# Optimization experiments

Measured on AMD Instinct MI355X. Metric: run time of the kernel, lower is better.

The kernel has to match this reference:

```python
import jax, jax.numpy as jnp
import numpy as np

B, N, D, H = 2, 2048, 1024, 16
DH = D // H  # 64


def setup_inputs() -> dict:
    key = jax.random.key(0)
    k1, k2, k3, k4, k5 = jax.random.split(key, 5)
    x = jax.random.normal(k1, (B, N, D), dtype=jnp.float32)
    # per-head kqv Linear weights, stacked: [H, D, 3*DH] (acts as x @ W)
    W_kqv = jax.random.normal(k2, (H, D, 3 * DH), dtype=jnp.float32) * 0.02
    b_kqv = jax.random.normal(k3, (H, 3 * DH), dtype=jnp.float32) * 0.02
    W_proj = jax.random.normal(k4, (D, D), dtype=jnp.float32) * 0.02
    b_proj = jax.random.normal(k5, (D,), dtype=jnp.float32) * 0.02
    return {"x": x, "W_kqv": W_kqv, "b_kqv": b_kqv, "W_proj": W_proj, "b_proj": b_proj}


def reference(x, W_kqv, b_kqv, W_proj, b_proj):
    # per-head projections, all heads batched: [B, H, N, 3*DH]
    kqv = jnp.einsum('bnd,hde->bhne', x, W_kqv) + b_kqv[None, :, None, :]
    # original chunk order is k, q, v
    k, q, v = jnp.split(kqv, 3, axis=-1)  # each [B, H, N, DH]
    # scores: A = q @ k^T / sqrt(DH)  -> [B, H, N, N]
    A = jnp.einsum('bhnd,bhmd->bhnm', q, k) / jnp.sqrt(jnp.asarray(DH, x.dtype))
    causal = jnp.tril(jnp.ones((N, N), dtype=bool))
    A = jnp.where(causal[None, None, :, :], A, -jnp.inf)
    attn = jax.nn.softmax(A, axis=-1)
    sa = jnp.einsum('bhnm,bhmd->bhnd', attn, v)          # [B, H, N, DH]
    sa = sa.transpose(0, 2, 1, 3).reshape(B, N, D)        # concat heads
    out = sa @ W_proj.T + b_proj                          # output projection
    return out
```

## Files before the change

kernel.cpp:

```cpp
#include <hip/hip_runtime.h>
#include <hip/hip_bf16.h>
#include <cstdint>
#include <cstddef>

#define B_  2
#define N_  2048
#define D_  1024
#define H_  16
#define DH_ 64
#define E3_ 192

typedef __attribute__((ext_vector_type(8))) short short8;
typedef __attribute__((ext_vector_type(8))) unsigned short ushort8v;
typedef __attribute__((ext_vector_type(4))) float floatx4;

static __device__ __forceinline__ unsigned short f2bf(float f) {
  union { float f; unsigned u; } c; c.f = f;
  unsigned r = c.u + 0x7fffu + ((c.u >> 16) & 1u);
  return (unsigned short)(r >> 16);
}

#define MFMA(a,b,c) __builtin_amdgcn_mfma_f32_16x16x32_bf16((a),(b),(c),0,0,0)

#define GL_LDS16(g, l) __builtin_amdgcn_global_load_lds( \
    (const __attribute__((address_space(1))) void*)(g),  \
    (__attribute__((address_space(3))) void*)(l), 16, 0, 0)

__global__ __launch_bounds__(256) void k_f2bf(const float* __restrict__ in,
                                              unsigned short* __restrict__ out, int n8) {
  int i = blockIdx.x * blockDim.x + threadIdx.x;
  if (i >= n8) return;
  const float4* p = (const float4*)in + (size_t)i * 2;
  float4 a = p[0], b = p[1];
  ushort8v o;
  o[0]=f2bf(a.x); o[1]=f2bf(a.y); o[2]=f2bf(a.z); o[3]=f2bf(a.w);
  o[4]=f2bf(b.x); o[5]=f2bf(b.y); o[6]=f2bf(b.z); o[7]=f2bf(b.w);
  *((ushort8v*)out + i) = o;
}

__global__ __launch_bounds__(256) void k_twkqv(const float* __restrict__ W,
                                               unsigned short* __restrict__ Wt) {
  __shared__ float tile[64][65];
  int h = blockIdx.z, e0 = blockIdx.y * 64, d0 = blockIdx.x * 64;
  int t = threadIdx.x;
  const float* Wp = W + (size_t)h * D_ * E3_;
  int dr = t >> 2, ec = (t & 3) * 16;
#pragma unroll
  for (int j = 0; j < 16; j += 4) {
    float4 wv = *(const float4*)&Wp[(size_t)(d0 + dr) * E3_ + e0 + ec + j];
    tile[dr][ec + j + 0] = wv.x; tile[dr][ec + j + 1] = wv.y;
    tile[dr][ec + j + 2] = wv.z; tile[dr][ec + j + 3] = wv.w;
  }
  __syncthreads();
  int er = t >> 2, dc = (t & 3) * 16;
  ushort8v o0, o1;
#pragma unroll
  for (int j = 0; j < 8; j++) o0[j] = f2bf(tile[dc + j][er]);
#pragma unroll
  for (int j = 0; j < 8; j++) o1[j] = f2bf(tile[dc + 8 + j][er]);
  size_t o = ((size_t)h * E3_ + e0 + er) * D_ + d0 + dc;
  *(ushort8v*)&Wt[o]     = o0;
  *(ushort8v*)&Wt[o + 8] = o1;
}

__global__ __launch_bounds__(256) void k_qkv(const unsigned short* __restrict__ Xb,
                                             const unsigned short* __restrict__ Wt,
                                             const float* __restrict__ bkqv,
                                             unsigned short* __restrict__ Qb,
                                             unsigned short* __restrict__ Kb,
                                             unsigned short* __restrict__ Vt) {
  __shared__ unsigned short Alds[128 * 32];
  __shared__ unsigned short Blds[128 * 32];
  int t = threadIdx.x;
  int m0 = blockIdx.x * 128, c0 = blockIdx.y * 128;
  int wave = t >> 6, lane = t & 63, quad = lane >> 4, l16 = lane & 15;
  int wm = (wave >> 1) * 64, wn = (wave & 1) * 64;
  floatx4 acc[4][4];
#pragma unroll
  for (int i = 0; i < 4; i++)
#pragma unroll
    for (int j = 0; j < 4; j++) acc[i][j] = (floatx4){0.f, 0.f, 0.f, 0.f};

  const unsigned short* gA = Xb + (size_t)(m0 + wave * 32 + (lane >> 2)) * D_ + (lane & 3) * 8;
  const unsigned short* gB = Wt + (size_t)(c0 + wave * 32 + (lane >> 2)) * D_ + (lane & 3) * 8;
  unsigned short* lA = &Alds[(wave * 32) * 32];
  unsigned short* lB = &Blds[(wave * 32) * 32];

  for (int k0 = 0; k0 < D_; k0 += 32) {
    GL_LDS16(gA + k0,            lA);
    GL_LDS16(gA + k0 + 16 * D_,  lA + 16 * 32);
    GL_LDS16(gB + k0,            lB);
    GL_LDS16(gB + k0 + 16 * D_,  lB + 16 * 32);
    __syncthreads();
    short8 a[4], b[4];
#pragma unroll
    for (int mi = 0; mi < 4; mi++) a[mi] = *(const short8*)&Alds[(wm + mi * 16 + l16) * 32 + quad * 8];
#pragma unroll
    for (int ni = 0; ni < 4; ni++) b[ni] = *(const short8*)&Blds[(wn + ni * 16 + l16) * 32 + quad * 8];
#pragma unroll
    for (int mi = 0; mi < 4; mi++)
#pragma unroll
      for (int ni = 0; ni < 4; ni++) acc[mi][ni] = MFMA(a[mi], b[ni], acc[mi][ni]);
    __syncthreads();
  }

#pragma unroll
  for (int mi = 0; mi < 4; mi++)
#pragma unroll
    for (int ni = 0; ni < 4; ni++) {
      int col = c0 + wn + ni * 16 + l16;
      int h = col / 192;
      int e = col - h * 192;
      int grow = m0 + wm + mi * 16 + quad * 4;
      int b = grow >> 11, n0 = grow & (N_ - 1);
      int bh = b * H_ + h;
      float bias = bkqv[col];
      floatx4 v = acc[mi][ni];
      if (e < 64) {
        size_t base = ((size_t)bh * N_ + n0) * DH_ + e;
#pragma unroll
        for (int r = 0; r < 4; r++) Kb[base + (size_t)r * DH_] = f2bf(v[r] + bias);
      } else if (e < 128) {
        size_t base = ((size_t)bh * N_ + n0) * DH_ + (e - 64);
#pragma unroll
        for (int r = 0; r < 4; r++) Qb[base + (size_t)r * DH_] = f2bf((v[r] + bias) * 0.125f);
      } else {
        ushort4 pk;
        pk.x = f2bf(v[0] + bias); pk.y = f2bf(v[1] + bias);
        pk.z = f2bf(v[2] + bias); pk.w = f2bf(v[3] + bias);
        *(ushort4*)&Vt[((size_t)bh * DH_ + (e - 128)) * N_ + n0] = pk;
      }
    }
}

#define PSTR 72
__global__ __launch_bounds__(256) void k_flash(const unsigned short* __restrict__ Qb,
                                               const unsigned short* __restrict__ Kb,
                                               const unsigned short* __restrict__ Vt,
                                               unsigned short* __restrict__ sab) {
  int bh = blockIdx.x;
  int yr = blockIdx.y, g = yr >> 3, o = yr & 7;
  int qb = (g == 0) ? o : (g == 1) ? 31 - o : (g == 2) ? 8 + o : 23 - o;
  int q0b = qb * 64;
  int wave = threadIdx.x >> 6;
  int lane = threadIdx.x & 63, quad = lane >> 4, l16 = lane & 15;
  const unsigned short* Qp = Qb + (size_t)bh * N_ * DH_;
  const unsigned short* Kp = Kb + (size_t)bh * N_ * DH_;
  const unsigned short* Vp = Vt + (size_t)bh * DH_ * N_;
  __shared__ unsigned short Klds[2 * 64 * 32];
  __shared__ unsigned short Vlds[2 * 64 * 32];
  __shared__ unsigned short Plds[4][16 * PSTR];
  unsigned short* P = Plds[wave];

  int q0w = q0b + wave * 16;
  short8 qf0 = *(const short8*)&Qp[(q0w + l16) * DH_ + quad * 8];
  short8 qf1 = *(const short8*)&Qp[(q0w + l16) * DH_ + 32 + quad * 8];

  const unsigned short* gK = Kp + (size_t)(wave * 16 + (lane >> 2)) * DH_ + (lane & 3) * 8;
  const unsigned short* gV = Vp + (size_t)(wave * 16 + (lane >> 2)) * N_ + (lane & 3) * 8;
  unsigned short* lK = &Klds[(wave * 16) * 32];
  unsigned short* lV = &Vlds[(wave * 16) * 32];

  floatx4 O[4];
  float lr[4];
#pragma unroll
  for (int r = 0; r < 4; r++) { O[r] = (floatx4){0.f, 0.f, 0.f, 0.f}; lr[r] = 0.f; }

  for (int kv0 = 0; kv0 <= q0b; kv0 += 64) {
    GL_LDS16(gK + (size_t)kv0 * DH_,      lK);
    GL_LDS16(gK + (size_t)kv0 * DH_ + 32, lK + 64 * 32);
    GL_LDS16(gV + kv0,                    lV);
    GL_LDS16(gV + kv0 + 32,               lV + 64 * 32);
    __syncthreads();

    short8 kf[4][2], vf[4][2];
#pragma unroll
    for (int c = 0; c < 4; c++) {
      kf[c][0] = *(const short8*)&Klds[(c * 16 + l16) * 32 + quad * 8];
      kf[c][1] = *(const short8*)&Klds[(64 + c * 16 + l16) * 32 + quad * 8];
    }
#pragma unroll
    for (int dt = 0; dt < 4; dt++) {
      vf[dt][0] = *(const short8*)&Vlds[(dt * 16 + l16) * 32 + quad * 8];
      vf[dt][1] = *(const short8*)&Vlds[(64 + dt * 16 + l16) * 32 + quad * 8];
    }
    floatx4 s[4];
#pragma unroll
    for (int c = 0; c < 4; c++) {
      s[c] = (floatx4){0.f, 0.f, 0.f, 0.f};
      s[c] = MFMA(qf0, kf[c][0], s[c]);
      s[c] = MFMA(qf1, kf[c][1], s[c]);
    }
    if (kv0 == q0b) {
#pragma unroll
      for (int c = 0; c < 4; c++)
#pragma unroll
        for (int r = 0; r < 4; r++) {
          int row = wave * 16 + quad * 4 + r;
          if (c * 16 + l16 > row) s[c][r] = -1e30f;
        }
    }
#pragma unroll
    for (int c = 0; c < 4; c++)
#pragma unroll
      for (int r = 0; r < 4; r++)
        s[c][r] = __builtin_amdgcn_exp2f(s[c][r] * 1.44269504f);
#pragma unroll
    for (int r = 0; r < 4; r++)
      lr[r] += (s[0][r] + s[1][r]) + (s[2][r] + s[3][r]);
#pragma unroll
    for (int c = 0; c < 4; c++)
#pragma unroll
      for (int r = 0; r < 4; r++)
        P[(quad * 4 + r) * PSTR + c * 16 + l16] = f2bf(s[c][r]);
    __asm__ volatile("s_waitcnt lgkmcnt(0)" ::: "memory");
    short8 pa0 = *(const short8*)&P[l16 * PSTR + quad * 8];
    short8 pa1 = *(const short8*)&P[l16 * PSTR + 32 + quad * 8];
#pragma unroll
    for (int dt = 0; dt < 4; dt++) {
      O[dt] = MFMA(pa0, vf[dt][0], O[dt]);
      O[dt] = MFMA(pa1, vf[dt][1], O[dt]);
    }
    __syncthreads();
  }
#pragma unroll
  for (int m = 1; m < 16; m <<= 1)
#pragma unroll
    for (int r = 0; r < 4; r++) lr[r] += __shfl_xor(lr[r], m);

  int b = bh >> 4, h = bh & 15;
#pragma unroll
  for (int r = 0; r < 4; r++) {
    float inv = 1.0f / lr[r];
    size_t base = ((size_t)b * N_ + q0w + quad * 4 + r) * D_ + h * DH_;
#pragma unroll
    for (int dt = 0; dt < 4; dt++) sab[base + dt * 16 + l16] = f2bf(O[dt][r] * inv);
  }
}

__global__ __launch_bounds__(256) void k_proj(const unsigned short* __restrict__ sab,
                                              const unsigned short* __restrict__ Wpb,
                                              const float* __restrict__ bproj,
                                              float* __restrict__ out) {
  __shared__ unsigned short Alds[128 * 32];
  __shared__ unsigned short Blds[64 * 32];
  int t = threadIdx.x;
  int m0 = blockIdx.x * 128, c0 = blockIdx.y * 64;
  int wave = t >> 6, lane = t & 63, quad = lane >> 4, l16 = lane & 15;
  int wm = (wave >> 1) * 64, wn = (wave & 1) * 32;
  floatx4 acc[4][2];
#pragma unroll
  for (int i = 0; i < 4; i++) { acc[i][0] = (floatx4){0,0,0,0}; acc[i][1] = (floatx4){0,0,0,0}; }

  const unsigned short* gA = sab + (size_t)(m0 + wave * 32 + (lane >> 2)) * D_ + (lane & 3) * 8;
  const unsigned short* gB = Wpb + (size_t)(c0 + wave * 16 + (lane >> 2)) * D_ + (lane & 3) * 8;
  unsigned short* lA = &Alds[(wave * 32) * 32];
  unsigned short* lB = &Blds[(wave * 16) * 32];

  for (int k0 = 0; k0 < D_; k0 += 32) {
    GL_LDS16(gA + k0,           lA);
    GL_LDS16(gA + k0 + 16 * D_, lA + 16 * 32);
    GL_LDS16(gB + k0,           lB);
    __syncthreads();
    short8 a[4], b[2];
#pragma unroll
    for (int mi = 0; mi < 4; mi++) a[mi] = *(const short8*)&Alds[(wm + mi * 16 + l16) * 32 + quad * 8];
#pragma unroll
    for (int ni = 0; ni < 2; ni++) b[ni] = *(const short8*)&Blds[(wn + ni * 16 + l16) * 32 + quad * 8];
#pragma unroll
    for (int mi = 0; mi < 4; mi++)
#pragma unroll
      for (int ni = 0; ni < 2; ni++) acc[mi][ni] = MFMA(a[mi], b[ni], acc[mi][ni]);
    __syncthreads();
  }
#pragma unroll
  for (int mi = 0; mi < 4; mi++)
#pragma unroll
    for (int ni = 0; ni < 2; ni++) {
      int col = c0 + wn + ni * 16 + l16;
      int grow = m0 + wm + mi * 16 + quad * 4;
      float bias = bproj[col];
#pragma unroll
      for (int r = 0; r < 4; r++)
        out[(size_t)(grow + r) * D_ + col] = acc[mi][ni][r] + bias;
    }
}

extern "C" void kernel_launch(void* const* d_in, const int* in_sizes, int n_in,
                              void* d_out, int out_size, void* d_ws, size_t ws_size,
                              hipStream_t stream) {
  const float* x     = (const float*)d_in[0];
  const float* Wkqv  = (const float*)d_in[1];
  const float* bkqv  = (const float*)d_in[2];
  const float* Wproj = (const float*)d_in[3];
  const float* bproj = (const float*)d_in[4];
  float* out = (float*)d_out;

  char* w = (char*)d_ws;
  unsigned short* Xb  = (unsigned short*)(w);
  unsigned short* Wt  = (unsigned short*)(w + (8u  << 20));
  unsigned short* Wpb = (unsigned short*)(w + (14u << 20));
  unsigned short* Qb  = (unsigned short*)(w + (16u << 20));
  unsigned short* Kb  = (unsigned short*)(w + (24u << 20));
  unsigned short* Vt  = (unsigned short*)(w + (32u << 20));
  unsigned short* sa  = (unsigned short*)(w + (40u << 20));

  k_f2bf<<<(B_ * N_ * D_ / 8 + 255) / 256, 256, 0, stream>>>(x, Xb, B_ * N_ * D_ / 8);
  k_twkqv<<<dim3(D_ / 64, E3_ / 64, H_), 256, 0, stream>>>(Wkqv, Wt);
  k_f2bf<<<(D_ * D_ / 8 + 255) / 256, 256, 0, stream>>>(Wproj, Wpb, D_ * D_ / 8);
  k_qkv<<<dim3(B_ * N_ / 128, 3072 / 128), 256, 0, stream>>>(Xb, Wt, bkqv, Qb, Kb, Vt);
  k_flash<<<dim3(B_ * H_, N_ / 64), 256, 0, stream>>>(Qb, Kb, Vt, sa);
  k_proj<<<dim3(B_ * N_ / 128, D_ / 64), 256, 0, stream>>>(sa, Wpb, bproj, out);
}
```

Measured before the change: 195.8 us.

## Regroup QKV weights by k/q/v, double K-step GEMMs, 128-row flash tiles

The K/Q/V weight transpose now writes columns grouped by category rather than per head. This lets the QKV GEMM epilogue branch once per block and replace the division by 192 with shifts. Both GEMMs now stage two 32-wide K slices per barrier pair, which halves the number of synchronizations. The flash kernel processes 128 query rows per block as two 64-row subtiles that share each loaded K/V tile, which halves K/V traffic per query. The cost is higher register pressure, fewer flash blocks, and a simpler causal load-balancing order.

```diff
diff --git a/kernel.cpp b/kernel.cpp
--- a/kernel.cpp
+++ b/kernel.cpp
@@ -41,7 +41,7 @@
 __global__ __launch_bounds__(256) void k_twkqv(const float* __restrict__ W,
                                                unsigned short* __restrict__ Wt) {
   __shared__ float tile[64][65];
-  int h = blockIdx.z, e0 = blockIdx.y * 64, d0 = blockIdx.x * 64;
+  int h = blockIdx.z, cat = blockIdx.y, e0 = cat * 64, d0 = blockIdx.x * 64;
   int t = threadIdx.x;
   const float* Wp = W + (size_t)h * D_ * E3_;
   int dr = t >> 2, ec = (t & 3) * 16;
@@ -58,7 +58,7 @@
   for (int j = 0; j < 8; j++) o0[j] = f2bf(tile[dc + j][er]);
 #pragma unroll
   for (int j = 0; j < 8; j++) o1[j] = f2bf(tile[dc + 8 + j][er]);
-  size_t o = ((size_t)h * E3_ + e0 + er) * D_ + d0 + dc;
+  size_t o = ((size_t)(cat * 1024 + h * 64 + er)) * D_ + d0 + dc;
   *(ushort8v*)&Wt[o]     = o0;
   *(ushort8v*)&Wt[o + 8] = o1;
 }
@@ -69,8 +69,8 @@
                                              unsigned short* __restrict__ Qb,
                                              unsigned short* __restrict__ Kb,
                                              unsigned short* __restrict__ Vt) {
-  __shared__ unsigned short Alds[128 * 32];
-  __shared__ unsigned short Blds[128 * 32];
+  __shared__ unsigned short Alds[2][128 * 32];
+  __shared__ unsigned short Blds[2][128 * 32];
   int t = threadIdx.x;
   int m0 = blockIdx.x * 128, c0 = blockIdx.y * 128;
   int wave = t >> 6, lane = t & 63, quad = lane >> 4, l16 = lane & 15;
@@ -83,52 +83,62 @@
 
   const unsigned short* gA = Xb + (size_t)(m0 + wave * 32 + (lane >> 2)) * D_ + (lane & 3) * 8;
   const unsigned short* gB = Wt + (size_t)(c0 + wave * 32 + (lane >> 2)) * D_ + (lane & 3) * 8;
-  unsigned short* lA = &Alds[(wave * 32) * 32];
-  unsigned short* lB = &Blds[(wave * 32) * 32];
-
-  for (int k0 = 0; k0 < D_; k0 += 32) {
-    GL_LDS16(gA + k0,            lA);
-    GL_LDS16(gA + k0 + 16 * D_,  lA + 16 * 32);
-    GL_LDS16(gB + k0,            lB);
-    GL_LDS16(gB + k0 + 16 * D_,  lB + 16 * 32);
-    __syncthreads();
-    short8 a[4], b[4];
-#pragma unroll
-    for (int mi = 0; mi < 4; mi++) a[mi] = *(const short8*)&Alds[(wm + mi * 16 + l16) * 32 + quad * 8];
-#pragma unroll
-    for (int ni = 0; ni < 4; ni++) b[ni] = *(const short8*)&Blds[(wn + ni * 16 + l16) * 32 + quad * 8];
-#pragma unroll
-    for (int mi = 0; mi < 4; mi++)
-#pragma unroll
-      for (int ni = 0; ni < 4; ni++) acc[mi][ni] = MFMA(a[mi], b[ni], acc[mi][ni]);
-    __syncthreads();
-  }
-
+  unsigned short* lA0 = &Alds[0][(wave * 32) * 32];
+  unsigned short* lA1 = &Alds[1][(wave * 32) * 32];
+  unsigned short* lB0 = &Blds[0][(wave * 32) * 32];
+  unsigned short* lB1 = &Blds[1][(wave * 32) * 32];
+
+  for (int k0 = 0; k0 < D_; k0 += 64) {
+    GL_LDS16(gA + k0,                 lA0);
+    GL_LDS16(gA + k0 + 16 * D_,       lA0 + 16 * 32);
+    GL_LDS16(gA + k0 + 32,            lA1);
+    GL_LDS16(gA + k0 + 32 + 16 * D_,  lA1 + 16 * 32);
+    GL_LDS16(gB + k0,                 lB0);
+    GL_LDS16(gB + k0 + 16 * D_,       lB0 + 16 * 32);
+    GL_LDS16(gB + k0 + 32,            lB1);
+    GL_LDS16(gB + k0 + 32 + 16 * D_,  lB1 + 16 * 32);
+    __syncthreads();
+#pragma unroll
+    for (int kk = 0; kk < 2; kk++) {
+      short8 a[4], b[4];
+#pragma unroll
+      for (int mi = 0; mi < 4; mi++) a[mi] = *(const short8*)&Alds[kk][(wm + mi * 16 + l16) * 32 + quad * 8];
+#pragma unroll
+      for (int ni = 0; ni < 4; ni++) b[ni] = *(const short8*)&Blds[kk][(wn + ni * 16 + l16) * 32 + quad * 8];
+#pragma unroll
+      for (int mi = 0; mi < 4; mi++)
+#pragma unroll
+        for (int ni = 0; ni < 4; ni++) acc[mi][ni] = MFMA(a[mi], b[ni], acc[mi][ni]);
+    }
+    __syncthreads();
+  }
+
+  int cat = c0 >> 10;
 #pragma unroll
   for (int mi = 0; mi < 4; mi++)
 #pragma unroll
     for (int ni = 0; ni < 4; ni++) {
-      int col = c0 + wn + ni * 16 + l16;
-      int h = col / 192;
-      int e = col - h * 192;
+      int colp = c0 + wn + ni * 16 + l16;
+      int h = (colp >> 6) & 15;
+      int e = colp & 63;
       int grow = m0 + wm + mi * 16 + quad * 4;
       int b = grow >> 11, n0 = grow & (N_ - 1);
       int bh = b * H_ + h;
-      float bias = bkqv[col];
+      float bias = bkqv[h * E3_ + cat * 64 + e];
       floatx4 v = acc[mi][ni];
-      if (e < 64) {
+      if (cat == 0) {
         size_t base = ((size_t)bh * N_ + n0) * DH_ + e;
 #pragma unroll
         for (int r = 0; r < 4; r++) Kb[base + (size_t)r * DH_] = f2bf(v[r] + bias);
-      } else if (e < 128) {
-        size_t base = ((size_t)bh * N_ + n0) * DH_ + (e - 64);
+      } else if (cat == 1) {
+        size_t base = ((size_t)bh * N_ + n0) * DH_ + e;
 #pragma unroll
         for (int r = 0; r < 4; r++) Qb[base + (size_t)r * DH_] = f2bf((v[r] + bias) * 0.125f);
       } else {
         ushort4 pk;
         pk.x = f2bf(v[0] + bias); pk.y = f2bf(v[1] + bias);
         pk.z = f2bf(v[2] + bias); pk.w = f2bf(v[3] + bias);
-        *(ushort4*)&Vt[((size_t)bh * DH_ + (e - 128)) * N_ + n0] = pk;
+        *(ushort4*)&Vt[((size_t)bh * DH_ + e) * N_ + n0] = pk;
       }
     }
 }
@@ -139,9 +149,9 @@
                                                const unsigned short* __restrict__ Vt,
                                                unsigned short* __restrict__ sab) {
   int bh = blockIdx.x;
-  int yr = blockIdx.y, g = yr >> 3, o = yr & 7;
-  int qb = (g == 0) ? o : (g == 1) ? 31 - o : (g == 2) ? 8 + o : 23 - o;
-  int q0b = qb * 64;
+  int y = blockIdx.y;
+  int qb = (y < 8) ? y : 23 - y;
+  int q0b = qb * 128;
   int wave = threadIdx.x >> 6;
   int lane = threadIdx.x & 63, quad = lane >> 4, l16 = lane & 15;
   const unsigned short* Qp = Qb + (size_t)bh * N_ * DH_;
@@ -152,89 +162,102 @@
   __shared__ unsigned short Plds[4][16 * PSTR];
   unsigned short* P = Plds[wave];
 
-  int q0w = q0b + wave * 16;
-  short8 qf0 = *(const short8*)&Qp[(q0w + l16) * DH_ + quad * 8];
-  short8 qf1 = *(const short8*)&Qp[(q0w + l16) * DH_ + 32 + quad * 8];
-
+  short8 qf[2][2];
+#pragma unroll
+  for (int st = 0; st < 2; st++) {
+    int q0 = q0b + st * 64 + wave * 16;
+    qf[st][0] = *(const short8*)&Qp[(q0 + l16) * DH_ + quad * 8];
+    qf[st][1] = *(const short8*)&Qp[(q0 + l16) * DH_ + 32 + quad * 8];
+  }
   const unsigned short* gK = Kp + (size_t)(wave * 16 + (lane >> 2)) * DH_ + (lane & 3) * 8;
   const unsigned short* gV = Vp + (size_t)(wave * 16 + (lane >> 2)) * N_ + (lane & 3) * 8;
   unsigned short* lK = &Klds[(wave * 16) * 32];
   unsigned short* lV = &Vlds[(wave * 16) * 32];
 
-  floatx4 O[4];
-  float lr[4];
-#pragma unroll
-  for (int r = 0; r < 4; r++) { O[r] = (floatx4){0.f, 0.f, 0.f, 0.f}; lr[r] = 0.f; }
-
-  for (int kv0 = 0; kv0 <= q0b; kv0 += 64) {
+  floatx4 O[2][4];
+  float lr[2][4];
+#pragma unroll
+  for (int st = 0; st < 2; st++)
+#pragma unroll
+    for (int r = 0; r < 4; r++) { O[st][r] = (floatx4){0.f, 0.f, 0.f, 0.f}; lr[st][r] = 0.f; }
+
+  for (int kv0 = 0; kv0 <= q0b + 64; kv0 += 64) {
     GL_LDS16(gK + (size_t)kv0 * DH_,      lK);
     GL_LDS16(gK + (size_t)kv0 * DH_ + 32, lK + 64 * 32);
     GL_LDS16(gV + kv0,                    lV);
     GL_LDS16(gV + kv0 + 32,               lV + 64 * 32);
     __syncthreads();
 
-    short8 kf[4][2], vf[4][2];
+    short8 kf0[4], kf1[4], vf0[4], vf1[4];
 #pragma unroll
     for (int c = 0; c < 4; c++) {
-      kf[c][0] = *(const short8*)&Klds[(c * 16 + l16) * 32 + quad * 8];
-      kf[c][1] = *(const short8*)&Klds[(64 + c * 16 + l16) * 32 + quad * 8];
-    }
-#pragma unroll
-    for (int dt = 0; dt < 4; dt++) {
-      vf[dt][0] = *(const short8*)&Vlds[(dt * 16 + l16) * 32 + quad * 8];
-      vf[dt][1] = *(const short8*)&Vlds[(64 + dt * 16 + l16) * 32 + quad * 8];
-    }
-    floatx4 s[4];
-#pragma unroll
-    for (int c = 0; c < 4; c++) {
-      s[c] = (floatx4){0.f, 0.f, 0.f, 0.f};
-      s[c] = MFMA(qf0, kf[c][0], s[c]);
-      s[c] = MFMA(qf1, kf[c][1], s[c]);
-    }
-    if (kv0 == q0b) {
+      kf0[c] = *(const short8*)&Klds[(c * 16 + l16) * 32 + quad * 8];
+      kf1[c] = *(const short8*)&Klds[(64 + c * 16 + l16) * 32 + quad * 8];
+      vf0[c] = *(const short8*)&Vlds[(c * 16 + l16) * 32 + quad * 8];
+      vf1[c] = *(const short8*)&Vlds[(64 + c * 16 + l16) * 32 + quad * 8];
+    }
+#pragma unroll
+    for (int st = 0; st < 2; st++) {
+      if (st == 0 && kv0 > q0b) continue;
+      floatx4 s[4];
+#pragma unroll
+      for (int c = 0; c < 4; c++) {
+        s[c] = (floatx4){0.f, 0.f, 0.f, 0.f};
+        s[c] = MFMA(qf[st][0], kf0[c], s[c]);
+        s[c] = MFMA(qf[st][1], kf1[c], s[c]);
+      }
+      if (kv0 == q0b + st * 64) {
+#pragma unroll
+        for (int c = 0; c < 4; c++)
+#pragma unroll
+          for (int r = 0; r < 4; r++) {
+            int row = wave * 16 + quad * 4 + r;
+            if (c * 16 + l16 > row) s[c][r] = -1e30f;
+          }
+      }
 #pragma unroll
       for (int c = 0; c < 4; c++)
 #pragma unroll
-        for (int r = 0; r < 4; r++) {
-          int row = wave * 16 + quad * 4 + r;
-          if (c * 16 + l16 > row) s[c][r] = -1e30f;
-        }
-    }
-#pragma unroll
-    for (int c = 0; c < 4; c++)
+        for (int r = 0; r < 4; r++)
+          s[c][r] = __builtin_amdgcn_exp2f(s[c][r] * 1.44269504f);
 #pragma unroll
       for (int r = 0; r < 4; r++)
-        s[c][r] = __builtin_amdgcn_exp2f(s[c][r] * 1.44269504f);
-#pragma unroll
-    for (int r = 0; r < 4; r++)
-      lr[r] += (s[0][r] + s[1][r]) + (s[2][r] + s[3][r]);
-#pragma unroll
-    for (int c = 0; c < 4; c++)
-#pragma unroll
-      for (int r = 0; r < 4; r++)
-        P[(quad * 4 + r) * PSTR + c * 16 + l16] = f2bf(s[c][r]);
-    __asm__ volatile("s_waitcnt lgkmcnt(0)" ::: "memory");
-    short8 pa0 = *(const short8*)&P[l16 * PSTR + quad * 8];
-    short8 pa1 = *(const short8*)&P[l16 * PSTR + 32 + quad * 8];
-#pragma unroll
-    for (int dt = 0; dt < 4; dt++) {
-      O[dt] = MFMA(pa0, vf[dt][0], O[dt]);
-      O[dt] = MFMA(pa1, vf[dt][1], O[dt]);
+        lr[st][r] += (s[0][r] + s[1][r]) + (s[2][r] + s[3][r]);
+#pragma unroll
+      for (int c = 0; c < 4; c++)
+#pragma unroll
+        for (int r = 0; r < 4; r++)
+          P[(quad * 4 + r) * PSTR + c * 16 + l16] = f2bf(s[c][r]);
+      __asm__ volatile("s_waitcnt lgkmcnt(0)" ::: "memory");
+      short8 pa0 = *(const short8*)&P[l16 * PSTR + quad * 8];
+      short8 pa1 = *(const short8*)&P[l16 * PSTR + 32 + quad * 8];
+      __asm__ volatile("" ::: "memory");
+#pragma unroll
+      for (int dt = 0; dt < 4; dt++) {
+        O[st][dt] = MFMA(pa0, vf0[dt], O[st][dt]);
+        O[st][dt] = MFMA(pa1, vf1[dt], O[st][dt]);
+      }
     }
     __syncthreads();
   }
 #pragma unroll
   for (int m = 1; m < 16; m <<= 1)
 #pragma unroll
-    for (int r = 0; r < 4; r++) lr[r] += __shfl_xor(lr[r], m);
+    for (int st = 0; st < 2; st++)
+#pragma unroll
+      for (int r = 0; r < 4; r++) lr[st][r] += __shfl_xor(lr[st][r], m);
 
   int b = bh >> 4, h = bh & 15;
 #pragma unroll
-  for (int r = 0; r < 4; r++) {
-    float inv = 1.0f / lr[r];
-    size_t base = ((size_t)b * N_ + q0w + quad * 4 + r) * D_ + h * DH_;
-#pragma unroll
-    for (int dt = 0; dt < 4; dt++) sab[base + dt * 16 + l16] = f2bf(O[dt][r] * inv);
+  for (int st = 0; st < 2; st++) {
+    int q0 = q0b + st * 64 + wave * 16;
+#pragma unroll
+    for (int r = 0; r < 4; r++) {
+      float inv = 1.0f / lr[st][r];
+      size_t base = ((size_t)b * N_ + q0 + quad * 4 + r) * D_ + h * DH_;
+#pragma unroll
+      for (int dt = 0; dt < 4; dt++) sab[base + dt * 16 + l16] = f2bf(O[st][dt][r] * inv);
+    }
   }
 }
 
@@ -242,8 +265,8 @@
                                               const unsigned short* __restrict__ Wpb,
                                               const float* __restrict__ bproj,
                                               float* __restrict__ out) {
-  __shared__ unsigned short Alds[128 * 32];
-  __shared__ unsigned short Blds[64 * 32];
+  __shared__ unsigned short Alds[2][128 * 32];
+  __shared__ unsigned short Blds[2][64 * 32];
   int t = threadIdx.x;
   int m0 = blockIdx.x * 128, c0 = blockIdx.y * 64;
   int wave = t >> 6, lane = t & 63, quad = lane >> 4, l16 = lane & 15;
@@ -254,23 +277,31 @@
 
   const unsigned short* gA = sab + (size_t)(m0 + wave * 32 + (lane >> 2)) * D_ + (lane & 3) * 8;
   const unsigned short* gB = Wpb + (size_t)(c0 + wave * 16 + (lane >> 2)) * D_ + (lane & 3) * 8;
-  unsigned short* lA = &Alds[(wave * 32) * 32];
-  unsigned short* lB = &Blds[(wave * 16) * 32];
-
-  for (int k0 = 0; k0 < D_; k0 += 32) {
-    GL_LDS16(gA + k0,           lA);
-    GL_LDS16(gA + k0 + 16 * D_, lA + 16 * 32);
-    GL_LDS16(gB + k0,           lB);
-    __syncthreads();
-    short8 a[4], b[2];
-#pragma unroll
-    for (int mi = 0; mi < 4; mi++) a[mi] = *(const short8*)&Alds[(wm + mi * 16 + l16) * 32 + quad * 8];
-#pragma unroll
-    for (int ni = 0; ni < 2; ni++) b[ni] = *(const short8*)&Blds[(wn + ni * 16 + l16) * 32 + quad * 8];
-#pragma unroll
-    for (int mi = 0; mi < 4; mi++)
-#pragma unroll
-      for (int ni = 0; ni < 2; ni++) acc[mi][ni] = MFMA(a[mi], b[ni], acc[mi][ni]);
+  unsigned short* lA0 = &Alds[0][(wave * 32) * 32];
+  unsigned short* lA1 = &Alds[1][(wave * 32) * 32];
+  unsigned short* lB0 = &Blds[0][(wave * 16) * 32];
+  unsigned short* lB1 = &Blds[1][(wave * 16) * 32];
+
+  for (int k0 = 0; k0 < D_; k0 += 64) {
+    GL_LDS16(gA + k0,                lA0);
+    GL_LDS16(gA + k0 + 16 * D_,      lA0 + 16 * 32);
+    GL_LDS16(gA + k0 + 32,           lA1);
+    GL_LDS16(gA + k0 + 32 + 16 * D_, lA1 + 16 * 32);
+    GL_LDS16(gB + k0,                lB0);
+    GL_LDS16(gB + k0 + 32,           lB1);
+    __syncthreads();
+#pragma unroll
+    for (int kk = 0; kk < 2; kk++) {
+      short8 a[4], b[2];
+#pragma unroll
+      for (int mi = 0; mi < 4; mi++) a[mi] = *(const short8*)&Alds[kk][(wm + mi * 16 + l16) * 32 + quad * 8];
+#pragma unroll
+      for (int ni = 0; ni < 2; ni++) b[ni] = *(const short8*)&Blds[kk][(wn + ni * 16 + l16) * 32 + quad * 8];
+#pragma unroll
+      for (int mi = 0; mi < 4; mi++)
+#pragma unroll
+        for (int ni = 0; ni < 2; ni++) acc[mi][ni] = MFMA(a[mi], b[ni], acc[mi][ni]);
+    }
     __syncthreads();
   }
 #pragma unroll
@@ -306,9 +337,9 @@
   unsigned short* sa  = (unsigned short*)(w + (40u << 20));
 
   k_f2bf<<<(B_ * N_ * D_ / 8 + 255) / 256, 256, 0, stream>>>(x, Xb, B_ * N_ * D_ / 8);
-  k_twkqv<<<dim3(D_ / 64, E3_ / 64, H_), 256, 0, stream>>>(Wkqv, Wt);
+  k_twkqv<<<dim3(D_ / 64, 3, H_), 256, 0, stream>>>(Wkqv, Wt);
   k_f2bf<<<(D_ * D_ / 8 + 255) / 256, 256, 0, stream>>>(Wproj, Wpb, D_ * D_ / 8);
   k_qkv<<<dim3(B_ * N_ / 128, 3072 / 128), 256, 0, stream>>>(Xb, Wt, bkqv, Qb, Kb, Vt);
-  k_flash<<<dim3(B_ * H_, N_ / 64), 256, 0, stream>>>(Qb, Kb, Vt, sa);
+  k_flash<<<dim3(B_ * H_, N_ / 128), 256, 0, stream>>>(Qb, Kb, Vt, sa);
   k_proj<<<dim3(B_ * N_ / 128, D_ / 64), 256, 0, stream>>>(sa, Wpb, bproj, out);
 }
```

Result: slower. 207.5 us (+6.0%).
